# Kernel optimization log

Hardware: AMD Instinct MI355X
Metric: run time of the kernel (lower is better)

Reference implementation:

```python
import jax, jax.numpy as jnp
import numpy as np

# Module hyperparameters (init_kwargs)
OSFREQ = 8.0      # oversampling_frequency
MAXFREQ = 1.0     # maximum_frequency
PERIOD = 1.0      # sampling_period
THRESH = 0.0      # thresh


def _periodogram_cfg(n_samples):
    """Angular frequencies and sample times for the oversampled periodogram."""
    timespan = PERIOD * (n_samples + 1) - 1
    all_samples = PERIOD * jnp.arange(1, n_samples + 1, dtype=jnp.float32)  # (T,)
    freqstep = 1.0 / (timespan * OSFREQ)
    n_freqs = int(np.floor((MAXFREQ * n_samples / (2.0 * timespan)) / freqstep))
    angular_frequencies = (2.0 * np.pi * freqstep) * jnp.arange(
        1, n_freqs + 1, dtype=jnp.float32
    )  # (F,)
    return angular_frequencies, all_samples


def _fit_spectrum(basis_masked, data_masked):
    """Least-squares projection of observed data onto each (masked) basis fn.
    basis_masked: (B, F, T) zeroed at unseen frames; data_masked: (B, C, T)."""
    num = jnp.einsum('bft,bct->bfc', basis_masked, data_masked)
    den = (basis_masked ** 2).sum(-1)[..., None]  # (B, F, 1)
    spectrum = num / den
    if THRESH > 0:
        a = jnp.abs(spectrum)
        spectrum = jnp.where(a / a.max() <= THRESH, 0.0, spectrum)
    return spectrum  # (B, F, C)


def _spectral_interpolate(data, mask):
    # data: (B, C, T) float; mask: (B, 1, T) bool (True = observed)
    B, C, T = data.shape
    w = mask.astype(data.dtype)          # (B, 1, T)
    wt = w[:, 0, :]                      # (B, T)
    ang, t = _periodogram_cfg(T)         # (F,), (T,)
    arg = ang[:, None] * t[None, :]      # (F, T)

    # Per-frequency phase offset tau from observed timepoints only (mask-weighted)
    num = jnp.einsum('bt,ft->bf', wt, jnp.sin(2.0 * arg))
    den = jnp.einsum('bt,ft->bf', wt, jnp.cos(2.0 * arg))
    tau = jnp.arctan2(num, den) / (2.0 * ang)              # (B, F)

    shifted = arg[None, :, :] - (ang[None, :] * tau)[..., None]  # (B, F, T)
    sin_basis = jnp.sin(shifted)
    cos_basis = jnp.cos(shifted)
    sin_m = sin_basis * wt[:, None, :]   # basis restricted to observed frames
    cos_m = cos_basis * wt[:, None, :]
    data_m = data * w

    sin_spec = _fit_spectrum(sin_m, data_m)  # (B, F, C)
    cos_spec = _fit_spectrum(cos_m, data_m)

    # Reconstruct the full time series from the fitted spectrum
    recon = (jnp.einsum('bft,bfc->bct', sin_basis, sin_spec)
             + jnp.einsum('bft,bfc->bct', cos_basis, cos_spec))  # (B, C, T)

    # Normalise: match per-channel std over observed frames (unbiased)
    n_obs = wt.sum(-1)[:, None]          # (B, 1)
    def wstd(x):
        m = (x * w).sum(-1) / n_obs                               # (B, C)
        v = (((x - m[..., None]) ** 2) * w).sum(-1) / (n_obs - 1)
        return jnp.sqrt(v)
    norm_fac = wstd(recon) / wstd(data)  # (B, C)
    recon = recon / norm_fac[..., None]

    # Keep observed samples, fill censored frames with the reconstruction
    return jnp.where(mask, data, recon)


def setup_inputs() -> dict:
    key = jax.random.key(0)
    k1, k2 = jax.random.split(key)
    data = jax.random.normal(k1, (4, 512, 1024), dtype=jnp.float32)
    mask = jax.random.bernoulli(k2, 0.75, (4, 1, 1024))  # True = observed
    return {"data": data, "mask": mask}


def reference(data, mask):
    return _spectral_interpolate(data, mask)
```

## Files before the change

### kernel.cpp

```cpp
#include <hip/hip_runtime.h>
#include <hip/hip_bf16.h>
#include <hip/hip_fp16.h>

using bf16 = __hip_bfloat16;
typedef __attribute__((ext_vector_type(8))) short bf16x8;
typedef __attribute__((ext_vector_type(4))) short short4v;
typedef __attribute__((ext_vector_type(2))) short short2v;
typedef __attribute__((ext_vector_type(4))) float f32x4;
typedef __attribute__((ext_vector_type(2))) _Float16 halfx2;

#define C_2PI_8192 7.6699039394282072e-4f

static __device__ __forceinline__ short bf16bits(float v) {
  bf16 h = __float2bfloat16(v);
  return *reinterpret_cast<short*>(&h);
}

#define GLOAD(gp, lp)                                                          \
  __builtin_amdgcn_global_load_lds(                                            \
      (const __attribute__((address_space(1))) void*)(gp),                     \
      (__attribute__((address_space(3))) void*)(lp), 16, 0, 0)

__global__ __launch_bounds__(1024) void k_prep(const void* __restrict__ mask,
                                               float* __restrict__ wt,
                                               float* __restrict__ nobs,
                                               float* __restrict__ delta,
                                               float* __restrict__ invA) {
  __shared__ int cnt;
  __shared__ float wsum[16];
  int tid = threadIdx.x;
  if (tid == 0) cnt = 0;
  __syncthreads();
  const unsigned char* mb = (const unsigned char*)mask;
  int c = 0;
#pragma unroll
  for (int i = 0; i < 4; ++i) c += (mb[tid * 4 + i] != 0) ? 1 : 0;
  atomicAdd(&cnt, c);
  __syncthreads();
  bool bytemode = (cnt > 2048);
  const int* mi = (const int*)mask;
  float s = 0.f;
#pragma unroll
  for (int i = 0; i < 4; ++i) {
    int e = tid * 4 + i;
    bool on = bytemode ? (mb[e] != 0) : (mi[e] != 0);
    float w = on ? 1.0f : 0.0f;
    wt[e] = w;
    s += w;
  }
#pragma unroll
  for (int m = 32; m; m >>= 1) s += __shfl_xor(s, m, 64);
  int wid = tid >> 6, lane = tid & 63;
  if (lane == 0) wsum[wid] = s;
  __syncthreads();
  if (tid < 4) nobs[tid] = wsum[tid * 4] + wsum[tid * 4 + 1] + wsum[tid * 4 + 2] + wsum[tid * 4 + 3];
  __syncthreads();
  if (tid < 256) {
    const float W = (float)(6.283185307179586 / 8192.0);
    const float ang = W * 4096.0f;
    int b = tid >> 6;
    const float* wp = wt + (b << 10);
    float num = 0.f, den = 0.f;
    for (int t = lane; t < 1024; t += 64) {
      float tf = (float)(t + 1);
      float arg = ang * tf;
      float w = wp[t];
      num += w * sinf(2.0f * arg);
      den += w * cosf(2.0f * arg);
    }
#pragma unroll
    for (int m = 32; m; m >>= 1) {
      num += __shfl_xor(num, m, 64);
      den += __shfl_xor(den, m, 64);
    }
    float tau = atan2f(num, den) / (2.0f * ang);
    float P = ang * tau;
    float dss = 0.f;
    for (int t = lane; t < 1024; t += 64) {
      float tf = (float)(t + 1);
      float arg = ang * tf;
      float d = sinf(arg - P);
      delta[(b << 10) + t] = d;
      dss += wp[t] * d * d;
    }
#pragma unroll
    for (int m = 32; m; m >>= 1) dss += __shfl_xor(dss, m, 64);
    if (lane == 0) invA[b] = 1.f / dss;
  }
}

__global__ void k_build(bf16* __restrict__ AE, bf16* __restrict__ Be) {
  int bid = blockIdx.x;
  int region = bid >> 10;
  int idx = (bid & 1023) * 256 + threadIdx.x;
  short4v lo, hi;
  if (region < 2) {
    int r = idx >> 6, j8 = (idx & 63) << 3;
    int m = (r & 2047) + 1;
    bool is_sin = (r < 2048);
    int ph0 = (region == 0) ? ((m * (2 * j8 + 2)) & 8191) : ((m * (2 * j8 + 1)) & 8191);
    int step = (2 * m) & 8191;
    float s = __sinf(ph0 * C_2PI_8192), c = __cosf(ph0 * C_2PI_8192);
    float sr = __sinf(step * C_2PI_8192), cr = __cosf(step * C_2PI_8192);
#pragma unroll
    for (int j = 0; j < 8; ++j) {
      float v = is_sin ? s : c;
      if (j < 4) lo[j] = bf16bits(v); else hi[j - 4] = bf16bits(v);
      float ns = s * cr + c * sr;
      c = c * cr - s * sr;
      s = ns;
    }
    short* dst = (short*)AE + (size_t)region * 2097152 + ((size_t)r << 9) + j8;
    *(short4v*)dst = lo;
    *(short4v*)(dst + 4) = hi;
  } else {
    int jr = idx >> 9, k8 = (idx & 511) << 3;
    int tau = (region == 2) ? (2 * jr + 2) : (2 * jr + 1);
    int m0 = (k8 & 2047) + 1;
    bool is_sin = (k8 < 2048);
    int ph0 = (m0 * tau) & 8191;
    float s = __sinf(ph0 * C_2PI_8192), c = __cosf(ph0 * C_2PI_8192);
    float sr = __sinf(tau * C_2PI_8192), cr = __cosf(tau * C_2PI_8192);
#pragma unroll
    for (int j = 0; j < 8; ++j) {
      float v = is_sin ? s : c;
      if (j < 4) lo[j] = bf16bits(v); else hi[j - 4] = bf16bits(v);
      float ns = s * cr + c * sr;
      c = c * cr - s * sr;
      s = ns;
    }
    short* dst = (short*)Be + (size_t)(region - 2) * 2097152 + ((size_t)jr << 12) + k8;
    *(short4v*)dst = lo;
    *(short4v*)(dst + 4) = hi;
  }
}

__global__ __launch_bounds__(256) void k_mid(const float* __restrict__ wt,
                                             const float* __restrict__ nobs,
                                             const float* __restrict__ data,
                                             const float* __restrict__ delta,
                                             const float* __restrict__ invA,
                                             float4* __restrict__ scal,
                                             bf16* __restrict__ dmE,
                                             float* __restrict__ sdv,
                                             float* __restrict__ sd2v,
                                             float* __restrict__ ss4095,
                                             float* __restrict__ cs4096) {
  int bid = blockIdx.x, tid = threadIdx.x;
  int wid = tid >> 6, lane = tid & 63;
  if (bid < 2048) {
    int gw = bid * 4 + wid;
    int b = gw >> 11, f = gw & 2047;
    float num = 0.f, den = 0.f;
    int f2 = 2 * (f + 1);
    {
      int ph0 = (f2 * (lane + 1)) & 8191;
      int st = (f2 << 6) & 8191;
      float s = __sinf(ph0 * C_2PI_8192), c = __cosf(ph0 * C_2PI_8192);
      float sr = __sinf(st * C_2PI_8192), cr = __cosf(st * C_2PI_8192);
      const float* wp = wt + (b << 10) + lane;
#pragma unroll
      for (int i = 0; i < 16; ++i) {
        float w = wp[i << 6];
        num += w * s;
        den += w * c;
        float ns = s * cr + c * sr;
        c = c * cr - s * sr;
        s = ns;
      }
    }
#pragma unroll
    for (int m = 32; m; m >>= 1) {
      num += __shfl_xor(num, m, 64);
      den += __shfl_xor(den, m, 64);
    }
    if (lane == 0) {
      float th = 0.5f * atan2f(num, den);
      float c = cosf(th), s = sinf(th);
      float nb = nobs[b];
      float WSS = 0.5f * (nb - den);
      float WCC = 0.5f * (nb + den);
      float WSC = 0.5f * num;
      float den_s = c * c * WSS - 2.f * c * s * WSC + s * s * WCC;
      float den_c = c * c * WCC + 2.f * c * s * WSC + s * s * WSS;
      scal[gw] = make_float4(c, s, 1.f / den_s, 1.f / den_c);
    }
  } else {
    int bc = bid - 2048, b = bc >> 9;
    bf16* dmO = dmE + (1 << 20);
    size_t base = (size_t)bc * 1024 + tid * 4;
    float4 d4 = *(const float4*)(data + base);
    float4 w4 = *(const float4*)(wt + (b << 10) + tid * 4);
    float4 e4 = *(const float4*)(delta + (b << 10) + tid * 4);
    const float* d = (const float*)&d4;
    const float* w = (const float*)&w4;
    const float* e = (const float*)&e4;
    float wd[4];
    float sd = 0.f, sd2 = 0.f, sdd = 0.f, sdc = 0.f;
#pragma unroll
    for (int j = 0; j < 4; ++j) {
      wd[j] = w[j] * d[j];
      sd += wd[j];
      sd2 += wd[j] * d[j];
      sdd += wd[j] * e[j];
      sdc += (j & 1) ? wd[j] : -wd[j];
    }
    short2v dE, dO;
    dO[0] = bf16bits(wd[0]); dE[0] = bf16bits(wd[1]);
    dO[1] = bf16bits(wd[2]); dE[1] = bf16bits(wd[3]);
    *(short2v*)((short*)dmE + (size_t)bc * 512 + tid * 2) = dE;
    *(short2v*)((short*)dmO + (size_t)bc * 512 + tid * 2) = dO;
#pragma unroll
    for (int m = 32; m; m >>= 1) {
      sd += __shfl_xor(sd, m, 64);
      sd2 += __shfl_xor(sd2, m, 64);
      sdd += __shfl_xor(sdd, m, 64);
      sdc += __shfl_xor(sdc, m, 64);
    }
    __shared__ float red[4][4];
    if (lane == 0) { red[wid][0] = sd; red[wid][1] = sd2; red[wid][2] = sdd; red[wid][3] = sdc; }
    __syncthreads();
    if (tid == 0) {
      float a0 = 0, a1 = 0, a2 = 0, a3 = 0;
#pragma unroll
      for (int ww = 0; ww < 4; ++ww) { a0 += red[ww][0]; a1 += red[ww][1]; a2 += red[ww][2]; a3 += red[ww][3]; }
      sdv[bc] = a0;
      sd2v[bc] = a1;
      ss4095[bc] = a2 * invA[b];
      cs4096[bc] = a3 / nobs[b];
    }
  }
}

__global__ __launch_bounds__(256, 2) void k_gemm1_pq(const bf16* __restrict__ dmE,
                                                     const bf16* __restrict__ AE,
                                                     const float4* __restrict__ scal,
                                                     bf16* __restrict__ PQe,
                                                     bf16* __restrict__ PQo) {
  __shared__ bf16 As[128 * 64];
  __shared__ bf16 Bs[128 * 64];
  int bid = blockIdx.x;
  int swz = ((bid & 7) << 6) | (bid >> 3);
  int mt = swz & 15, ft = swz >> 4;
  int m0 = mt << 7, f0 = ft << 6;
  int tid = threadIdx.x, lane = tid & 63, wid = tid >> 6;
  int wm = (wid >> 1) << 6, wn = (wid & 1) << 6;
  int fr = lane & 15, kh = lane >> 4;

  int r0 = tid >> 3;
  int scol = ((tid & 7) ^ (r0 & 7)) << 3;
  const bf16* pa0 = dmE + (size_t)(m0 + r0) * 512 + scol;
  const bf16* pb[4];
#pragma unroll
  for (int n = 0; n < 4; ++n) {
    int row = n * 32 + r0;
    int gr = ((row >> 4) & 1) * 2048 + f0 + (row & 15) + ((row >> 5) << 4);
    pb[n] = AE + (size_t)gr * 512 + scol;
  }
  char* lA = (char*)As + (wid << 10);
  char* lB = (char*)Bs + (wid << 10);

  f32x4 accU[4][4] = {};
  f32x4 accV[4][4] = {};
  int sw = fr & 7;

#define K_BODY(ACC)                                                              \
  for (int kt = 0; kt < 8; ++kt) {                                               \
    _Pragma("unroll")                                                            \
    for (int n = 0; n < 4; ++n) {                                                \
      GLOAD(pa0 + n * 16384, lA + n * 4096);                                     \
      GLOAD(pb[n], lB + n * 4096);                                               \
      pb[n] += 64;                                                               \
    }                                                                            \
    pa0 += 64;                                                                   \
    __syncthreads();                                                             \
    _Pragma("unroll")                                                            \
    for (int s = 0; s < 2; ++s) {                                                \
      bf16x8 a[4];                                                               \
      _Pragma("unroll")                                                          \
      for (int i = 0; i < 4; ++i)                                                \
        a[i] = *(const bf16x8*)&As[(wm + i * 16 + fr) * 64 + ((((s << 2) + kh) ^ sw) << 3)]; \
      _Pragma("unroll")                                                          \
      for (int j = 0; j < 4; ++j) {                                              \
        bf16x8 bb = *(const bf16x8*)&Bs[(wn + j * 16 + fr) * 64 + ((((s << 2) + kh) ^ sw) << 3)]; \
        _Pragma("unroll")                                                        \
        for (int i = 0; i < 4; ++i)                                              \
          ACC[i][j] = __builtin_amdgcn_mfma_f32_16x16x32_bf16(a[i], bb, ACC[i][j], 0, 0, 0); \
      }                                                                          \
    }                                                                            \
    __syncthreads();                                                             \
  }

  K_BODY(accU)
  pa0 += (1 << 20) - 512;
#pragma unroll
  for (int n = 0; n < 4; ++n) pb[n] += (2 << 20) - 512;
  K_BODY(accV)
#undef K_BODY

  int b = m0 >> 9;
  short* pqe = (short*)PQe;
  short* pqo = (short*)PQo;
#pragma unroll
  for (int p = 0; p < 2; ++p) {
    int mi = f0 + (wn >> 1) + (p << 4) + fr;
    float4 sc = scal[(b << 11) + mi];
    float c = sc.x, s = sc.y, ids = sc.z, idc = sc.w;
    bool self = (mi == 2047);
#pragma unroll
    for (int i = 0; i < 4; ++i) {
#pragma unroll
      for (int q = 0; q < 4; ++q) {
        int bc = m0 + wm + i * 16 + (kh << 2) + q;
        float US = accU[i][2 * p][q], UC = accU[i][2 * p + 1][q];
        float VS = accV[i][2 * p][q], VC = accV[i][2 * p + 1][q];
        float Gs = US + VS, Gc = UC + VC;
        float gs = VS - US, gc = UC - VC;
        float ss = (c * Gs - s * Gc) * ids;
        float cs = (c * Gc + s * Gs) * idc;
        float P = c * ss + s * cs;
        float Q = c * cs - s * ss;
        float ssp = (c * gs + s * gc) * ids;
        float csp = (c * gc - s * gs) * idc;
        float Pp = self ? 0.f : (c * ssp - s * csp);
        float Qp = self ? 0.f : (c * csp + s * ssp);
        size_t base = (size_t)bc * 4096 + mi;
        pqe[base] = bf16bits(P - Pp);
        pqe[base + 2048] = bf16bits(Q + Qp);
        pqo[base] = bf16bits(P + Pp);
        pqo[base + 2048] = bf16bits(Q - Qp);
      }
    }
  }
}

__global__ __launch_bounds__(256, 4) void k_gemm2(const bf16* __restrict__ PQe,
                                                  const bf16* __restrict__ Be,
                                                  _Float16* __restrict__ Pe) {
  __shared__ bf16 As[128 * 64];
  __shared__ bf16 Bs[128 * 64];
  int bid = blockIdx.x;
  int swz = ((bid & 7) << 6) | (bid >> 3);
  int eo = swz >> 8;
  int slice = (swz >> 6) & 3;
  int tl = swz & 63;
  int mt = tl & 15, nt = tl >> 4;
  int m0 = mt << 7, n0 = nt << 7;
  int tid = threadIdx.x, lane = tid & 63, wid = tid >> 6;
  int wm = (wid >> 1) << 6, wn = (wid & 1) << 6;
  int fr = lane & 15, kh = lane >> 4;

  const bf16* A = PQe + (size_t)eo * (8 << 20);
  const bf16* B = Be + (size_t)eo * (2 << 20);
  _Float16* C = Pe + (size_t)eo * (8 << 20);

  int r0 = tid >> 3;
  int scol = ((tid & 7) ^ (r0 & 7)) << 3;
  const bf16* pa0 = A + (size_t)slice * 1024 + (size_t)(m0 + r0) * 4096 + scol;
  const bf16* pb0 = B + (size_t)slice * 1024 + (size_t)(n0 + r0) * 4096 + scol;
  _Float16* Cp = C + (size_t)slice * 1048576;
  char* lA = (char*)As + (wid << 10);
  char* lB = (char*)Bs + (wid << 10);

  f32x4 acc[4][4] = {};
  int sw = fr & 7;

  for (int kt = 0; kt < 16; ++kt) {
#pragma unroll
    for (int n = 0; n < 4; ++n) {
      GLOAD(pa0 + n * 131072, lA + n * 4096);
      GLOAD(pb0 + n * 131072, lB + n * 4096);
    }
    pa0 += 64; pb0 += 64;
    __syncthreads();
#pragma unroll
    for (int s = 0; s < 2; ++s) {
      bf16x8 a[4];
#pragma unroll
      for (int i = 0; i < 4; ++i)
        a[i] = *(const bf16x8*)&As[(wm + i * 16 + fr) * 64 + ((((s << 2) + kh) ^ sw) << 3)];
#pragma unroll
      for (int j = 0; j < 4; ++j) {
        bf16x8 bb = *(const bf16x8*)&Bs[(wn + j * 16 + fr) * 64 + ((((s << 2) + kh) ^ sw) << 3)];
#pragma unroll
        for (int i = 0; i < 4; ++i)
          acc[i][j] = __builtin_amdgcn_mfma_f32_16x16x32_bf16(a[i], bb, acc[i][j], 0, 0, 0);
      }
    }
    __syncthreads();
  }
#pragma unroll
  for (int i = 0; i < 4; ++i) {
#pragma unroll
    for (int q = 0; q < 4; ++q) {
      size_t row = m0 + wm + i * 16 + (kh << 2) + q;
      _Float16* cp = Cp + row * 512 + n0 + wn + fr;
#pragma unroll
      for (int j = 0; j < 4; ++j) cp[j * 16] = (_Float16)acc[i][j][q];
    }
  }
}

__global__ __launch_bounds__(256) void k_tail(const _Float16* __restrict__ Pe,
                                              const _Float16* __restrict__ Po,
                                              const float* __restrict__ data,
                                              const float* __restrict__ wt,
                                              const float* __restrict__ delta,
                                              const float* __restrict__ ss4095,
                                              const float* __restrict__ cs4096,
                                              const float* __restrict__ sdv,
                                              const float* __restrict__ sd2v,
                                              const float* __restrict__ nobs,
                                              float* __restrict__ out) {
  int bc = blockIdx.x, b = bc >> 9, tid = threadIdx.x;
  size_t base = (size_t)bc * 1024 + tid * 4;
  int jj = tid * 2;
  float r[4] = {0.f, 0.f, 0.f, 0.f};
#pragma unroll
  for (int s = 0; s < 4; ++s) {
    halfx2 pe = *(const halfx2*)(Pe + (size_t)s * 1048576 + (size_t)bc * 512 + jj);
    halfx2 po = *(const halfx2*)(Po + (size_t)s * 1048576 + (size_t)bc * 512 + jj);
    r[0] += (float)po[0];
    r[1] += (float)pe[0];
    r[2] += (float)po[1];
    r[3] += (float)pe[1];
  }
  float ssv = ss4095[bc], csv = cs4096[bc];
  float4 e4 = *(const float4*)(delta + (b << 10) + tid * 4);
  float4 w4 = *(const float4*)(wt + (b << 10) + tid * 4);
  float4 d4 = *(const float4*)(data + base);
  const float* e = (const float*)&e4;
  const float* w = (const float*)&w4;
  const float* d = (const float*)&d4;
  float sr = 0.f, sr2 = 0.f;
#pragma unroll
  for (int j = 0; j < 4; ++j) {
    r[j] += e[j] * ssv + ((j & 1) ? csv : -csv);
    float wr = w[j] * r[j];
    sr += wr;
    sr2 += wr * r[j];
  }
#pragma unroll
  for (int m = 32; m; m >>= 1) {
    sr += __shfl_xor(sr, m, 64);
    sr2 += __shfl_xor(sr2, m, 64);
  }
  __shared__ float red[4][2];
  __shared__ float s_inv;
  int wid = tid >> 6, lane = tid & 63;
  if (lane == 0) { red[wid][0] = sr; red[wid][1] = sr2; }
  __syncthreads();
  if (tid == 0) {
    float a0 = 0, a1 = 0;
#pragma unroll
    for (int ww = 0; ww < 4; ++ww) { a0 += red[ww][0]; a1 += red[ww][1]; }
    float n = nobs[b];
    float mr = a0 / n, vr = (a1 - n * mr * mr) / (n - 1.f);
    float md = sdv[bc] / n, vd = (sd2v[bc] - n * md * md) / (n - 1.f);
    s_inv = sqrtf(vd / vr);
  }
  __syncthreads();
  float inv = s_inv;
  float4 o;
  ((float*)&o)[0] = (w[0] != 0.f) ? d[0] : r[0] * inv;
  ((float*)&o)[1] = (w[1] != 0.f) ? d[1] : r[1] * inv;
  ((float*)&o)[2] = (w[2] != 0.f) ? d[2] : r[2] * inv;
  ((float*)&o)[3] = (w[3] != 0.f) ? d[3] : r[3] * inv;
  *(float4*)(out + base) = o;
}

extern "C" void kernel_launch(void* const* d_in, const int* in_sizes, int n_in,
                              void* d_out, int out_size, void* d_ws, size_t ws_size,
                              hipStream_t stream) {
  const float* data = (const float*)d_in[0];
  const void* mask = d_in[1];
  float* out = (float*)d_out;
  char* ws = (char*)d_ws;

  float* wt = (float*)(ws);
  float* nobs = (float*)(ws + 16384);
  float* invA = (float*)(ws + 16640);
  float* sdv = (float*)(ws + 17408);
  float* sd2v = (float*)(ws + 25600);
  float* ss4095 = (float*)(ws + 33792);
  float* cs4096 = (float*)(ws + 41984);
  float* delta = (float*)(ws + 50176);
  float4* scal = (float4*)(ws + 131072);
  const size_t MB = 1ull << 20;
  bf16* AE = (bf16*)(ws + 1 * MB);
  bf16* Be = (bf16*)(ws + 9 * MB);
  bf16* dmE = (bf16*)(ws + 17 * MB);
  bf16* PQe = (bf16*)(ws + 21 * MB);
  bf16* PQo = (bf16*)(ws + 37 * MB);
  _Float16* Pe = (_Float16*)(ws + 53 * MB);
  _Float16* Po = (_Float16*)(ws + 69 * MB);

  k_prep<<<1, 1024, 0, stream>>>(mask, wt, nobs, delta, invA);
  k_build<<<4096, 256, 0, stream>>>(AE, Be);
  k_mid<<<4096, 256, 0, stream>>>(wt, nobs, data, delta, invA, scal, dmE, sdv, sd2v, ss4095, cs4096);
  k_gemm1_pq<<<512, 256, 0, stream>>>(dmE, AE, scal, PQe, PQo);
  k_gemm2<<<512, 256, 0, stream>>>(PQe, Be, Pe);
  k_tail<<<2048, 256, 0, stream>>>(Pe, Po, data, wt, delta, ss4095, cs4096, sdv, sd2v, nobs, out);
}
```

Before: 94.36 us.

## Fuse prep/build/mid into one kernel and use 8-wave GEMM blocks

Merges the single-block prep kernel, the basis build kernel and the mid kernel into one launch. Each block now reads the mask directly and detects its element width itself, instead of going through a precomputed weight array. The per-row data statistics move from the mid kernel into the tail kernel, so the serial one-block prep stage disappears and two launches are saved. Both GEMMs switch from 256 to 512 threads per block, with each wave owning a 64x32 tile instead of 64x64. This halves accumulator registers per thread, at the cost of redundant mask-width detection in every block.

```diff
diff --git a/kernel.cpp b/kernel.cpp
--- a/kernel.cpp
+++ b/kernel.cpp
@@ -21,50 +21,92 @@
       (const __attribute__((address_space(1))) void*)(gp),                     \
       (__attribute__((address_space(3))) void*)(lp), 16, 0, 0)
 
-__global__ __launch_bounds__(1024) void k_prep(const void* __restrict__ mask,
-                                               float* __restrict__ wt,
-                                               float* __restrict__ nobs,
-                                               float* __restrict__ delta,
-                                               float* __restrict__ invA) {
-  __shared__ int cnt;
-  __shared__ float wsum[16];
-  int tid = threadIdx.x;
-  if (tid == 0) cnt = 0;
-  __syncthreads();
-  const unsigned char* mb = (const unsigned char*)mask;
-  int c = 0;
-#pragma unroll
-  for (int i = 0; i < 4; ++i) c += (mb[tid * 4 + i] != 0) ? 1 : 0;
-  atomicAdd(&cnt, c);
-  __syncthreads();
-  bool bytemode = (cnt > 2048);
-  const int* mi = (const int*)mask;
-  float s = 0.f;
-#pragma unroll
-  for (int i = 0; i < 4; ++i) {
-    int e = tid * 4 + i;
-    bool on = bytemode ? (mb[e] != 0) : (mi[e] != 0);
-    float w = on ? 1.0f : 0.0f;
-    wt[e] = w;
-    s += w;
-  }
-#pragma unroll
-  for (int m = 32; m; m >>= 1) s += __shfl_xor(s, m, 64);
+#define DETECT_BYTEMODE(mask, tid, outvar)                                     \
+  __shared__ int _cnt;                                                         \
+  if ((tid) == 0) _cnt = 0;                                                    \
+  __syncthreads();                                                             \
+  {                                                                            \
+    const unsigned char* _mb = (const unsigned char*)(mask);                   \
+    int _c = 0;                                                                \
+    _Pragma("unroll")                                                          \
+    for (int _i = 0; _i < 16; ++_i) _c += (_mb[(tid) * 16 + _i] != 0) ? 1 : 0; \
+    atomicAdd(&_cnt, _c);                                                      \
+  }                                                                            \
+  __syncthreads();                                                             \
+  const bool outvar = (_cnt > 2048);
+
+static __device__ __forceinline__ float mask_w(const void* mask, bool bytemode, int e) {
+  if (bytemode) return (((const unsigned char*)mask)[e] != 0) ? 1.f : 0.f;
+  return (((const int*)mask)[e] != 0) ? 1.f : 0.f;
+}
+
+__global__ __launch_bounds__(256) void k_pre(const void* __restrict__ mask,
+                                             const float* __restrict__ data,
+                                             bf16* __restrict__ AE,
+                                             bf16* __restrict__ Be,
+                                             bf16* __restrict__ dmE,
+                                             float4* __restrict__ scal,
+                                             float* __restrict__ delta,
+                                             float* __restrict__ invA) {
+  int bid = blockIdx.x, tid = threadIdx.x;
+  if (bid < 4096) {
+    int region = bid >> 10;
+    int idx = (bid & 1023) * 256 + tid;
+    short4v lo, hi;
+    if (region < 2) {
+      int r = idx >> 6, j8 = (idx & 63) << 3;
+      int m = (r & 2047) + 1;
+      bool is_sin = (r < 2048);
+      int ph0 = (region == 0) ? ((m * (2 * j8 + 2)) & 8191) : ((m * (2 * j8 + 1)) & 8191);
+      int step = (2 * m) & 8191;
+      float s = __sinf(ph0 * C_2PI_8192), c = __cosf(ph0 * C_2PI_8192);
+      float sr = __sinf(step * C_2PI_8192), cr = __cosf(step * C_2PI_8192);
+#pragma unroll
+      for (int j = 0; j < 8; ++j) {
+        float v = is_sin ? s : c;
+        if (j < 4) lo[j] = bf16bits(v); else hi[j - 4] = bf16bits(v);
+        float ns = s * cr + c * sr;
+        c = c * cr - s * sr;
+        s = ns;
+      }
+      short* dst = (short*)AE + (size_t)region * 2097152 + ((size_t)r << 9) + j8;
+      *(short4v*)dst = lo;
+      *(short4v*)(dst + 4) = hi;
+    } else {
+      int jr = idx >> 9, k8 = (idx & 511) << 3;
+      int tau = (region == 2) ? (2 * jr + 2) : (2 * jr + 1);
+      int m0 = (k8 & 2047) + 1;
+      bool is_sin = (k8 < 2048);
+      int ph0 = (m0 * tau) & 8191;
+      float s = __sinf(ph0 * C_2PI_8192), c = __cosf(ph0 * C_2PI_8192);
+      float sr = __sinf(tau * C_2PI_8192), cr = __cosf(tau * C_2PI_8192);
+#pragma unroll
+      for (int j = 0; j < 8; ++j) {
+        float v = is_sin ? s : c;
+        if (j < 4) lo[j] = bf16bits(v); else hi[j - 4] = bf16bits(v);
+        float ns = s * cr + c * sr;
+        c = c * cr - s * sr;
+        s = ns;
+      }
+      short* dst = (short*)Be + (size_t)(region - 2) * 2097152 + ((size_t)jr << 12) + k8;
+      *(short4v*)dst = lo;
+      *(short4v*)(dst + 4) = hi;
+    }
+    return;
+  }
+  DETECT_BYTEMODE(mask, tid, bytemode)
   int wid = tid >> 6, lane = tid & 63;
-  if (lane == 0) wsum[wid] = s;
-  __syncthreads();
-  if (tid < 4) nobs[tid] = wsum[tid * 4] + wsum[tid * 4 + 1] + wsum[tid * 4 + 2] + wsum[tid * 4 + 3];
-  __syncthreads();
-  if (tid < 256) {
+  if (bid < 4100) {
+    int b = bid - 4096;
+    int base_b = b << 10;
     const float W = (float)(6.283185307179586 / 8192.0);
     const float ang = W * 4096.0f;
-    int b = tid >> 6;
-    const float* wp = wt + (b << 10);
+    __shared__ float red[4][2];
+    __shared__ float bc2[2];
     float num = 0.f, den = 0.f;
-    for (int t = lane; t < 1024; t += 64) {
-      float tf = (float)(t + 1);
-      float arg = ang * tf;
-      float w = wp[t];
+    for (int t = tid; t < 1024; t += 256) {
+      float arg = ang * (float)(t + 1);
+      float w = mask_w(mask, bytemode, base_b + t);
       num += w * sinf(2.0f * arg);
       den += w * cosf(2.0f * arg);
     }
@@ -73,97 +115,47 @@
       num += __shfl_xor(num, m, 64);
       den += __shfl_xor(den, m, 64);
     }
-    float tau = atan2f(num, den) / (2.0f * ang);
-    float P = ang * tau;
+    if (lane == 0) { red[wid][0] = num; red[wid][1] = den; }
+    __syncthreads();
+    if (tid == 0) {
+      float a0 = red[0][0] + red[1][0] + red[2][0] + red[3][0];
+      float a1 = red[0][1] + red[1][1] + red[2][1] + red[3][1];
+      float tau = atan2f(a0, a1) / (2.0f * ang);
+      bc2[0] = ang * tau;
+    }
+    __syncthreads();
+    float P = bc2[0];
     float dss = 0.f;
-    for (int t = lane; t < 1024; t += 64) {
-      float tf = (float)(t + 1);
-      float arg = ang * tf;
+    for (int t = tid; t < 1024; t += 256) {
+      float arg = ang * (float)(t + 1);
       float d = sinf(arg - P);
-      delta[(b << 10) + t] = d;
-      dss += wp[t] * d * d;
+      delta[base_b + t] = d;
+      float w = mask_w(mask, bytemode, base_b + t);
+      dss += w * d * d;
     }
 #pragma unroll
     for (int m = 32; m; m >>= 1) dss += __shfl_xor(dss, m, 64);
-    if (lane == 0) invA[b] = 1.f / dss;
-  }
-}
-
-__global__ void k_build(bf16* __restrict__ AE, bf16* __restrict__ Be) {
-  int bid = blockIdx.x;
-  int region = bid >> 10;
-  int idx = (bid & 1023) * 256 + threadIdx.x;
-  short4v lo, hi;
-  if (region < 2) {
-    int r = idx >> 6, j8 = (idx & 63) << 3;
-    int m = (r & 2047) + 1;
-    bool is_sin = (r < 2048);
-    int ph0 = (region == 0) ? ((m * (2 * j8 + 2)) & 8191) : ((m * (2 * j8 + 1)) & 8191);
-    int step = (2 * m) & 8191;
-    float s = __sinf(ph0 * C_2PI_8192), c = __cosf(ph0 * C_2PI_8192);
-    float sr = __sinf(step * C_2PI_8192), cr = __cosf(step * C_2PI_8192);
-#pragma unroll
-    for (int j = 0; j < 8; ++j) {
-      float v = is_sin ? s : c;
-      if (j < 4) lo[j] = bf16bits(v); else hi[j - 4] = bf16bits(v);
-      float ns = s * cr + c * sr;
-      c = c * cr - s * sr;
-      s = ns;
-    }
-    short* dst = (short*)AE + (size_t)region * 2097152 + ((size_t)r << 9) + j8;
-    *(short4v*)dst = lo;
-    *(short4v*)(dst + 4) = hi;
-  } else {
-    int jr = idx >> 9, k8 = (idx & 511) << 3;
-    int tau = (region == 2) ? (2 * jr + 2) : (2 * jr + 1);
-    int m0 = (k8 & 2047) + 1;
-    bool is_sin = (k8 < 2048);
-    int ph0 = (m0 * tau) & 8191;
-    float s = __sinf(ph0 * C_2PI_8192), c = __cosf(ph0 * C_2PI_8192);
-    float sr = __sinf(tau * C_2PI_8192), cr = __cosf(tau * C_2PI_8192);
-#pragma unroll
-    for (int j = 0; j < 8; ++j) {
-      float v = is_sin ? s : c;
-      if (j < 4) lo[j] = bf16bits(v); else hi[j - 4] = bf16bits(v);
-      float ns = s * cr + c * sr;
-      c = c * cr - s * sr;
-      s = ns;
-    }
-    short* dst = (short*)Be + (size_t)(region - 2) * 2097152 + ((size_t)jr << 12) + k8;
-    *(short4v*)dst = lo;
-    *(short4v*)(dst + 4) = hi;
-  }
-}
-
-__global__ __launch_bounds__(256) void k_mid(const float* __restrict__ wt,
-                                             const float* __restrict__ nobs,
-                                             const float* __restrict__ data,
-                                             const float* __restrict__ delta,
-                                             const float* __restrict__ invA,
-                                             float4* __restrict__ scal,
-                                             bf16* __restrict__ dmE,
-                                             float* __restrict__ sdv,
-                                             float* __restrict__ sd2v,
-                                             float* __restrict__ ss4095,
-                                             float* __restrict__ cs4096) {
-  int bid = blockIdx.x, tid = threadIdx.x;
-  int wid = tid >> 6, lane = tid & 63;
-  if (bid < 2048) {
-    int gw = bid * 4 + wid;
+    if (lane == 0) red[wid][0] = dss;
+    __syncthreads();
+    if (tid == 0)
+      invA[b] = 1.f / (red[0][0] + red[1][0] + red[2][0] + red[3][0]);
+  } else if (bid < 6148) {
+    int gw = (bid - 4100) * 4 + wid;
     int b = gw >> 11, f = gw & 2047;
-    float num = 0.f, den = 0.f;
+    int base_b = b << 10;
+    float num = 0.f, den = 0.f, nb = 0.f;
     int f2 = 2 * (f + 1);
     {
       int ph0 = (f2 * (lane + 1)) & 8191;
       int st = (f2 << 6) & 8191;
       float s = __sinf(ph0 * C_2PI_8192), c = __cosf(ph0 * C_2PI_8192);
       float sr = __sinf(st * C_2PI_8192), cr = __cosf(st * C_2PI_8192);
-      const float* wp = wt + (b << 10) + lane;
 #pragma unroll
       for (int i = 0; i < 16; ++i) {
-        float w = wp[i << 6];
+        float w = mask_w(mask, bytemode, base_b + lane + (i << 6));
         num += w * s;
         den += w * c;
+        nb += w;
         float ns = s * cr + c * sr;
         c = c * cr - s * sr;
         s = ns;
@@ -173,11 +165,11 @@
     for (int m = 32; m; m >>= 1) {
       num += __shfl_xor(num, m, 64);
       den += __shfl_xor(den, m, 64);
+      nb += __shfl_xor(nb, m, 64);
     }
     if (lane == 0) {
       float th = 0.5f * atan2f(num, den);
       float c = cosf(th), s = sinf(th);
-      float nb = nobs[b];
       float WSS = 0.5f * (nb - den);
       float WCC = 0.5f * (nb + den);
       float WSC = 0.5f * num;
@@ -186,53 +178,24 @@
       scal[gw] = make_float4(c, s, 1.f / den_s, 1.f / den_c);
     }
   } else {
-    int bc = bid - 2048, b = bc >> 9;
+    int bc = bid - 6148, b = bc >> 9;
     bf16* dmO = dmE + (1 << 20);
     size_t base = (size_t)bc * 1024 + tid * 4;
     float4 d4 = *(const float4*)(data + base);
-    float4 w4 = *(const float4*)(wt + (b << 10) + tid * 4);
-    float4 e4 = *(const float4*)(delta + (b << 10) + tid * 4);
     const float* d = (const float*)&d4;
-    const float* w = (const float*)&w4;
-    const float* e = (const float*)&e4;
+    int me = (b << 10) + tid * 4;
     float wd[4];
-    float sd = 0.f, sd2 = 0.f, sdd = 0.f, sdc = 0.f;
-#pragma unroll
-    for (int j = 0; j < 4; ++j) {
-      wd[j] = w[j] * d[j];
-      sd += wd[j];
-      sd2 += wd[j] * d[j];
-      sdd += wd[j] * e[j];
-      sdc += (j & 1) ? wd[j] : -wd[j];
-    }
+#pragma unroll
+    for (int j = 0; j < 4; ++j) wd[j] = mask_w(mask, bytemode, me + j) * d[j];
     short2v dE, dO;
     dO[0] = bf16bits(wd[0]); dE[0] = bf16bits(wd[1]);
     dO[1] = bf16bits(wd[2]); dE[1] = bf16bits(wd[3]);
     *(short2v*)((short*)dmE + (size_t)bc * 512 + tid * 2) = dE;
     *(short2v*)((short*)dmO + (size_t)bc * 512 + tid * 2) = dO;
-#pragma unroll
-    for (int m = 32; m; m >>= 1) {
-      sd += __shfl_xor(sd, m, 64);
-      sd2 += __shfl_xor(sd2, m, 64);
-      sdd += __shfl_xor(sdd, m, 64);
-      sdc += __shfl_xor(sdc, m, 64);
-    }
-    __shared__ float red[4][4];
-    if (lane == 0) { red[wid][0] = sd; red[wid][1] = sd2; red[wid][2] = sdd; red[wid][3] = sdc; }
-    __syncthreads();
-    if (tid == 0) {
-      float a0 = 0, a1 = 0, a2 = 0, a3 = 0;
-#pragma unroll
-      for (int ww = 0; ww < 4; ++ww) { a0 += red[ww][0]; a1 += red[ww][1]; a2 += red[ww][2]; a3 += red[ww][3]; }
-      sdv[bc] = a0;
-      sd2v[bc] = a1;
-      ss4095[bc] = a2 * invA[b];
-      cs4096[bc] = a3 / nobs[b];
-    }
-  }
-}
-
-__global__ __launch_bounds__(256, 2) void k_gemm1_pq(const bf16* __restrict__ dmE,
+  }
+}
+
+__global__ __launch_bounds__(512, 4) void k_gemm1_pq(const bf16* __restrict__ dmE,
                                                      const bf16* __restrict__ AE,
                                                      const float4* __restrict__ scal,
                                                      bf16* __restrict__ PQe,
@@ -244,35 +207,35 @@
   int mt = swz & 15, ft = swz >> 4;
   int m0 = mt << 7, f0 = ft << 6;
   int tid = threadIdx.x, lane = tid & 63, wid = tid >> 6;
-  int wm = (wid >> 1) << 6, wn = (wid & 1) << 6;
+  int wm = (wid >> 2) << 6, wn = (wid & 3) << 5;
   int fr = lane & 15, kh = lane >> 4;
 
   int r0 = tid >> 3;
   int scol = ((tid & 7) ^ (r0 & 7)) << 3;
   const bf16* pa0 = dmE + (size_t)(m0 + r0) * 512 + scol;
-  const bf16* pb[4];
-#pragma unroll
-  for (int n = 0; n < 4; ++n) {
-    int row = n * 32 + r0;
-    int gr = ((row >> 4) & 1) * 2048 + f0 + (row & 15) + ((row >> 5) << 4);
-    pb[n] = AE + (size_t)gr * 512 + scol;
+  const bf16* pb0;
+  const bf16* pb1;
+  {
+    int row0 = r0, row1 = 64 + r0;
+    int g0 = ((row0 >> 4) & 1) * 2048 + f0 + (row0 & 15) + ((row0 >> 5) << 4);
+    int g1 = ((row1 >> 4) & 1) * 2048 + f0 + (row1 & 15) + ((row1 >> 5) << 4);
+    pb0 = AE + (size_t)g0 * 512 + scol;
+    pb1 = AE + (size_t)g1 * 512 + scol;
   }
   char* lA = (char*)As + (wid << 10);
   char* lB = (char*)Bs + (wid << 10);
 
-  f32x4 accU[4][4] = {};
-  f32x4 accV[4][4] = {};
+  f32x4 accU[4][2] = {};
+  f32x4 accV[4][2] = {};
   int sw = fr & 7;
 
 #define K_BODY(ACC)                                                              \
   for (int kt = 0; kt < 8; ++kt) {                                               \
-    _Pragma("unroll")                                                            \
-    for (int n = 0; n < 4; ++n) {                                                \
-      GLOAD(pa0 + n * 16384, lA + n * 4096);                                     \
-      GLOAD(pb[n], lB + n * 4096);                                               \
-      pb[n] += 64;                                                               \
-    }                                                                            \
-    pa0 += 64;                                                                   \
+    GLOAD(pa0, lA);                                                              \
+    GLOAD(pa0 + 32768, lA + 8192);                                               \
+    GLOAD(pb0, lB);                                                              \
+    GLOAD(pb1, lB + 8192);                                                       \
+    pa0 += 64; pb0 += 64; pb1 += 64;                                             \
     __syncthreads();                                                             \
     _Pragma("unroll")                                                            \
     for (int s = 0; s < 2; ++s) {                                                \
@@ -281,7 +244,7 @@
       for (int i = 0; i < 4; ++i)                                                \
         a[i] = *(const bf16x8*)&As[(wm + i * 16 + fr) * 64 + ((((s << 2) + kh) ^ sw) << 3)]; \
       _Pragma("unroll")                                                          \
-      for (int j = 0; j < 4; ++j) {                                              \
+      for (int j = 0; j < 2; ++j) {                                              \
         bf16x8 bb = *(const bf16x8*)&Bs[(wn + j * 16 + fr) * 64 + ((((s << 2) + kh) ^ sw) << 3)]; \
         _Pragma("unroll")                                                        \
         for (int i = 0; i < 4; ++i)                                              \
@@ -293,27 +256,26 @@
 
   K_BODY(accU)
   pa0 += (1 << 20) - 512;
-#pragma unroll
-  for (int n = 0; n < 4; ++n) pb[n] += (2 << 20) - 512;
+  pb0 += (2 << 20) - 512;
+  pb1 += (2 << 20) - 512;
   K_BODY(accV)
 #undef K_BODY
 
   int b = m0 >> 9;
   short* pqe = (short*)PQe;
   short* pqo = (short*)PQo;
-#pragma unroll
-  for (int p = 0; p < 2; ++p) {
-    int mi = f0 + (wn >> 1) + (p << 4) + fr;
-    float4 sc = scal[(b << 11) + mi];
+  {
+    int f = f0 + (wn >> 1) + fr;
+    float4 sc = scal[(b << 11) + f];
     float c = sc.x, s = sc.y, ids = sc.z, idc = sc.w;
-    bool self = (mi == 2047);
+    bool self = (f == 2047);
 #pragma unroll
     for (int i = 0; i < 4; ++i) {
 #pragma unroll
       for (int q = 0; q < 4; ++q) {
         int bc = m0 + wm + i * 16 + (kh << 2) + q;
-        float US = accU[i][2 * p][q], UC = accU[i][2 * p + 1][q];
-        float VS = accV[i][2 * p][q], VC = accV[i][2 * p + 1][q];
+        float US = accU[i][0][q], UC = accU[i][1][q];
+        float VS = accV[i][0][q], VC = accV[i][1][q];
         float Gs = US + VS, Gc = UC + VC;
         float gs = VS - US, gc = UC - VC;
         float ss = (c * Gs - s * Gc) * ids;
@@ -324,7 +286,7 @@
         float csp = (c * gc - s * gs) * idc;
         float Pp = self ? 0.f : (c * ssp - s * csp);
         float Qp = self ? 0.f : (c * csp + s * ssp);
-        size_t base = (size_t)bc * 4096 + mi;
+        size_t base = (size_t)bc * 4096 + f;
         pqe[base] = bf16bits(P - Pp);
         pqe[base + 2048] = bf16bits(Q + Qp);
         pqo[base] = bf16bits(P + Pp);
@@ -334,7 +296,7 @@
   }
 }
 
-__global__ __launch_bounds__(256, 4) void k_gemm2(const bf16* __restrict__ PQe,
+__global__ __launch_bounds__(512, 4) void k_gemm2(const bf16* __restrict__ PQe,
                                                   const bf16* __restrict__ Be,
                                                   _Float16* __restrict__ Pe) {
   __shared__ bf16 As[128 * 64];
@@ -347,7 +309,7 @@
   int mt = tl & 15, nt = tl >> 4;
   int m0 = mt << 7, n0 = nt << 7;
   int tid = threadIdx.x, lane = tid & 63, wid = tid >> 6;
-  int wm = (wid >> 1) << 6, wn = (wid & 1) << 6;
+  int wm = (wid >> 2) << 6, wn = (wid & 3) << 5;
   int fr = lane & 15, kh = lane >> 4;
 
   const bf16* A = PQe + (size_t)eo * (8 << 20);
@@ -362,15 +324,14 @@
   char* lA = (char*)As + (wid << 10);
   char* lB = (char*)Bs + (wid << 10);
 
-  f32x4 acc[4][4] = {};
+  f32x4 acc[4][2] = {};
   int sw = fr & 7;
 
   for (int kt = 0; kt < 16; ++kt) {
-#pragma unroll
-    for (int n = 0; n < 4; ++n) {
-      GLOAD(pa0 + n * 131072, lA + n * 4096);
-      GLOAD(pb0 + n * 131072, lB + n * 4096);
-    }
+    GLOAD(pa0, lA);
+    GLOAD(pa0 + 262144, lA + 8192);
+    GLOAD(pb0, lB);
+    GLOAD(pb0 + 262144, lB + 8192);
     pa0 += 64; pb0 += 64;
     __syncthreads();
 #pragma unroll
@@ -380,7 +341,7 @@
       for (int i = 0; i < 4; ++i)
         a[i] = *(const bf16x8*)&As[(wm + i * 16 + fr) * 64 + ((((s << 2) + kh) ^ sw) << 3)];
 #pragma unroll
-      for (int j = 0; j < 4; ++j) {
+      for (int j = 0; j < 2; ++j) {
         bf16x8 bb = *(const bf16x8*)&Bs[(wn + j * 16 + fr) * 64 + ((((s << 2) + kh) ^ sw) << 3)];
 #pragma unroll
         for (int i = 0; i < 4; ++i)
@@ -396,7 +357,7 @@
       size_t row = m0 + wm + i * 16 + (kh << 2) + q;
       _Float16* cp = Cp + row * 512 + n0 + wn + fr;
 #pragma unroll
-      for (int j = 0; j < 4; ++j) cp[j * 16] = (_Float16)acc[i][j][q];
+      for (int j = 0; j < 2; ++j) cp[j * 16] = (_Float16)acc[i][j][q];
     }
   }
 }
@@ -404,15 +365,13 @@
 __global__ __launch_bounds__(256) void k_tail(const _Float16* __restrict__ Pe,
                                               const _Float16* __restrict__ Po,
                                               const float* __restrict__ data,
-                                              const float* __restrict__ wt,
+                                              const void* __restrict__ mask,
                                               const float* __restrict__ delta,
-                                              const float* __restrict__ ss4095,
-                                              const float* __restrict__ cs4096,
-                                              const float* __restrict__ sdv,
-                                              const float* __restrict__ sd2v,
-                                              const float* __restrict__ nobs,
+                                              const float* __restrict__ invA,
                                               float* __restrict__ out) {
   int bc = blockIdx.x, b = bc >> 9, tid = threadIdx.x;
+  DETECT_BYTEMODE(mask, tid, bytemode)
+  int wid = tid >> 6, lane = tid & 63;
   size_t base = (size_t)bc * 1024 + tid * 4;
   int jj = tid * 2;
   float r[4] = {0.f, 0.f, 0.f, 0.f};
@@ -425,13 +384,53 @@
     r[2] += (float)po[1];
     r[3] += (float)pe[1];
   }
-  float ssv = ss4095[bc], csv = cs4096[bc];
   float4 e4 = *(const float4*)(delta + (b << 10) + tid * 4);
-  float4 w4 = *(const float4*)(wt + (b << 10) + tid * 4);
   float4 d4 = *(const float4*)(data + base);
   const float* e = (const float*)&e4;
-  const float* w = (const float*)&w4;
   const float* d = (const float*)&d4;
+  float w[4];
+  int me = (b << 10) + tid * 4;
+#pragma unroll
+  for (int j = 0; j < 4; ++j) w[j] = mask_w(mask, bytemode, me + j);
+  float nbv = 0.f, sd = 0.f, sd2 = 0.f, sdd = 0.f, sdc = 0.f;
+#pragma unroll
+  for (int j = 0; j < 4; ++j) {
+    float wd = w[j] * d[j];
+    nbv += w[j];
+    sd += wd;
+    sd2 += wd * d[j];
+    sdd += wd * e[j];
+    sdc += (j & 1) ? wd : -wd;
+  }
+#pragma unroll
+  for (int m = 32; m; m >>= 1) {
+    nbv += __shfl_xor(nbv, m, 64);
+    sd += __shfl_xor(sd, m, 64);
+    sd2 += __shfl_xor(sd2, m, 64);
+    sdd += __shfl_xor(sdd, m, 64);
+    sdc += __shfl_xor(sdc, m, 64);
+  }
+  __shared__ float red[4][5];
+  __shared__ float bcast[3];
+  if (lane == 0) {
+    red[wid][0] = nbv; red[wid][1] = sd; red[wid][2] = sd2;
+    red[wid][3] = sdd; red[wid][4] = sdc;
+  }
+  __syncthreads();
+  if (tid == 0) {
+    float n = red[0][0] + red[1][0] + red[2][0] + red[3][0];
+    float a1 = red[0][1] + red[1][1] + red[2][1] + red[3][1];
+    float a2 = red[0][2] + red[1][2] + red[2][2] + red[3][2];
+    float a3 = red[0][3] + red[1][3] + red[2][3] + red[3][3];
+    float a4 = red[0][4] + red[1][4] + red[2][4] + red[3][4];
+    bcast[0] = a3 * invA[b];
+    bcast[1] = a4 / n;
+    float md = a1 / n;
+    bcast[2] = (a2 - n * md * md) / (n - 1.f);
+    red[0][0] = n;
+  }
+  __syncthreads();
+  float ssv = bcast[0], csv = bcast[1];
   float sr = 0.f, sr2 = 0.f;
 #pragma unroll
   for (int j = 0; j < 4; ++j) {
@@ -445,19 +444,16 @@
     sr += __shfl_xor(sr, m, 64);
     sr2 += __shfl_xor(sr2, m, 64);
   }
-  __shared__ float red[4][2];
+  __shared__ float red2[4][2];
   __shared__ float s_inv;
-  int wid = tid >> 6, lane = tid & 63;
-  if (lane == 0) { red[wid][0] = sr; red[wid][1] = sr2; }
+  if (lane == 0) { red2[wid][0] = sr; red2[wid][1] = sr2; }
   __syncthreads();
   if (tid == 0) {
-    float a0 = 0, a1 = 0;
-#pragma unroll
-    for (int ww = 0; ww < 4; ++ww) { a0 += red[ww][0]; a1 += red[ww][1]; }
-    float n = nobs[b];
+    float a0 = red2[0][0] + red2[1][0] + red2[2][0] + red2[3][0];
+    float a1 = red2[0][1] + red2[1][1] + red2[2][1] + red2[3][1];
+    float n = red[0][0];
     float mr = a0 / n, vr = (a1 - n * mr * mr) / (n - 1.f);
-    float md = sdv[bc] / n, vd = (sd2v[bc] - n * md * md) / (n - 1.f);
-    s_inv = sqrtf(vd / vr);
+    s_inv = sqrtf(bcast[2] / vr);
   }
   __syncthreads();
   float inv = s_inv;
@@ -477,13 +473,7 @@
   float* out = (float*)d_out;
   char* ws = (char*)d_ws;
 
-  float* wt = (float*)(ws);
-  float* nobs = (float*)(ws + 16384);
   float* invA = (float*)(ws + 16640);
-  float* sdv = (float*)(ws + 17408);
-  float* sd2v = (float*)(ws + 25600);
-  float* ss4095 = (float*)(ws + 33792);
-  float* cs4096 = (float*)(ws + 41984);
   float* delta = (float*)(ws + 50176);
   float4* scal = (float4*)(ws + 131072);
   const size_t MB = 1ull << 20;
@@ -495,10 +485,8 @@
   _Float16* Pe = (_Float16*)(ws + 53 * MB);
   _Float16* Po = (_Float16*)(ws + 69 * MB);
 
-  k_prep<<<1, 1024, 0, stream>>>(mask, wt, nobs, delta, invA);
-  k_build<<<4096, 256, 0, stream>>>(AE, Be);
-  k_mid<<<4096, 256, 0, stream>>>(wt, nobs, data, delta, invA, scal, dmE, sdv, sd2v, ss4095, cs4096);
-  k_gemm1_pq<<<512, 256, 0, stream>>>(dmE, AE, scal, PQe, PQo);
-  k_gemm2<<<512, 256, 0, stream>>>(PQe, Be, Pe);
-  k_tail<<<2048, 256, 0, stream>>>(Pe, Po, data, wt, delta, ss4095, cs4096, sdv, sd2v, nobs, out);
-}
+  k_pre<<<8196, 256, 0, stream>>>(mask, data, AE, Be, dmE, scal, delta, invA);
+  k_gemm1_pq<<<512, 512, 0, stream>>>(dmE, AE, scal, PQe, PQo);
+  k_gemm2<<<512, 512, 0, stream>>>(PQe, Be, Pe);
+  k_tail<<<2048, 256, 0, stream>>>(Pe, Po, data, mask, delta, invA, out);
+}
```

Measured after the change: 87.60 us. 7.2% less time.
